# Performance work log

Measured on AMD Instinct MI355X. Metric: run time of the kernel, lower is better.

The kernel has to match this reference:

```python
import jax, jax.numpy as jnp
import numpy as np

NUM_LAYERS = 4


def setup_inputs() -> dict:
    key = jax.random.key(0)
    k1, k2, k3, k4 = jax.random.split(key, 4)
    num_users, num_items, D, E = 100000, 50000, 64, 2000000
    N = num_users + num_items
    emb_users = jax.random.normal(k1, (num_users, D), dtype=jnp.float32)
    emb_items = jax.random.normal(k2, (num_items, D), dtype=jnp.float32)
    src = jax.random.randint(k3, (E,), 0, N, dtype=jnp.int64)
    dst = jax.random.randint(k4, (E,), 0, N, dtype=jnp.int64)
    edge_index = jnp.stack([src, dst], axis=0)
    return {"emb_users": emb_users, "emb_items": emb_items, "edge_index": edge_index}


def _lightgcn(emb_users, emb_items, edge_index):
    num_users = emb_users.shape[0]
    num_items = emb_items.shape[0]
    N = num_users + num_items
    src, dst = edge_index[0], edge_index[1]

    # gcn_norm without self-loops (PyG LGConv default): deg over destination nodes
    ones = jnp.ones(src.shape[0], dtype=emb_users.dtype)
    deg = jax.ops.segment_sum(ones, dst, num_segments=N)
    deg_inv_sqrt = jnp.where(deg > 0, jax.lax.rsqrt(jnp.maximum(deg, 1.0)), 0.0)
    norm = deg_inv_sqrt[src] * deg_inv_sqrt[dst]  # [E]

    emb = jnp.concatenate([emb_users, emb_items], axis=0)  # [N, D]
    acc = emb
    for _ in range(NUM_LAYERS):
        msg = norm[:, None] * emb[src]  # [E, D]
        emb = jax.ops.segment_sum(msg, dst, num_segments=N)
        acc = acc + emb

    # original: 1/(L+1) * mean(stack, dim=1) == sum / (L+1)^2
    emb_final = acc / float((NUM_LAYERS + 1) ** 2)
    return emb_final[:num_users], emb_final[num_users:]


def reference(emb_users, emb_items, edge_index):
    return _lightgcn(emb_users, emb_items, edge_index)
```

## Files before the change

kernel.cpp:

```cpp
#include <hip/hip_runtime.h>
#include <hip/hip_bf16.h>

#define D 64
#define NUM_LAYERS 4
#define TILE 4096
#define EPT 16
#define BKMAX 320


__global__ void cnt_kernel(const int* __restrict__ dst, int* __restrict__ cnt, int E) {
    int e = blockIdx.x * blockDim.x + threadIdx.x;
    if (e < E) atomicAdd(&cnt[dst[e]], 1);
}

__global__ void dis_kernel(const int* __restrict__ cnt, float* __restrict__ dis, int N) {
    int i = blockIdx.x * blockDim.x + threadIdx.x;
    if (i < N) {
        int c = cnt[i];
        dis[i] = (c > 0) ? rsqrtf((float)c) : 0.0f;
    }
}

__global__ void scan1_kernel(const int* __restrict__ cnt, int* __restrict__ excl,
                             int* __restrict__ partials, int N) {
    __shared__ int sm[256];
    int i = blockIdx.x * 256 + threadIdx.x;
    int v = (i < N) ? cnt[i] : 0;
    sm[threadIdx.x] = v;
    __syncthreads();
    for (int ofs = 1; ofs < 256; ofs <<= 1) {
        int t = (threadIdx.x >= ofs) ? sm[threadIdx.x - ofs] : 0;
        __syncthreads();
        sm[threadIdx.x] += t;
        __syncthreads();
    }
    if (i < N) excl[i] = sm[threadIdx.x] - v;
    if (threadIdx.x == 255) partials[blockIdx.x] = sm[255];
}

__global__ void scan2_kernel(int* __restrict__ partials, int nb) {
    __shared__ int sm[1024];
    int v = (threadIdx.x < nb) ? partials[threadIdx.x] : 0;
    sm[threadIdx.x] = v;
    __syncthreads();
    for (int ofs = 1; ofs < 1024; ofs <<= 1) {
        int t = (threadIdx.x >= ofs) ? sm[threadIdx.x - ofs] : 0;
        __syncthreads();
        sm[threadIdx.x] += t;
        __syncthreads();
    }
    if (threadIdx.x < nb) partials[threadIdx.x] = sm[threadIdx.x] - v;
}

__global__ void scan3_kernel(int* __restrict__ row_start, const int* __restrict__ partials,
                             int N, int E) {
    int i = blockIdx.x * 256 + threadIdx.x;
    if (i < N) row_start[i] += partials[blockIdx.x];
    if (i == 0) row_start[N] = E;
}

__global__ void gcur_init_kernel(const int* __restrict__ row_start, int* __restrict__ gcur, int nbk) {
    int b = blockIdx.x * blockDim.x + threadIdx.x;
    if (b < nbk) gcur[b] = row_start[b << 9];
}


__global__ __launch_bounds__(256) void placeA_kernel(const int* __restrict__ src,
                                                     const int* __restrict__ dst,
                                                     const float* __restrict__ dis,
                                                     int* __restrict__ gcur,
                                                     int2* __restrict__ mid,
                                                     int E, int nbk) {
    __shared__ int hist[BKMAX];
    __shared__ int gbase[BKMAX];
    int t = threadIdx.x;
    int tile0 = blockIdx.x * TILE;
    for (int i = t; i < nbk; i += 256) hist[i] = 0;
    __syncthreads();

    int   p_[EPT];
    float w_[EPT];
    int   b_[EPT];
    int   r_[EPT];
#pragma unroll
    for (int i = 0; i < EPT; ++i) {
        int e = tile0 + i * 256 + t;
        b_[i] = -1;
        if (e < E) {
            int s = src[e], d = dst[e];
            p_[i] = s | ((d & 511) << 18);
            w_[i] = dis[s] * dis[d];
            b_[i] = d >> 9;
            r_[i] = atomicAdd(&hist[b_[i]], 1);
        }
    }
    __syncthreads();
    for (int b = t; b < nbk; b += 256) {
        int h = hist[b];
        gbase[b] = (h > 0) ? atomicAdd(&gcur[b], h) : 0;
    }
    __syncthreads();
#pragma unroll
    for (int i = 0; i < EPT; ++i) {
        if (b_[i] >= 0) {
            int pos = gbase[b_[i]] + r_[i];
            mid[pos] = make_int2(p_[i], __float_as_int(w_[i]));
        }
    }
}

__global__ __launch_bounds__(256) void placeB_kernel(const int* __restrict__ row_start,
                                                     const int2* __restrict__ mid,
                                                     int2* __restrict__ csr,
                                                     int N, int nbk) {
    __shared__ int cur[512];
    int b = blockIdx.x;
    int t = threadIdx.x;
    int node0 = b << 9;
    int nend = min(512, N - node0);
    for (int i = t; i < nend; i += 256) cur[i] = row_start[node0 + i];
    __syncthreads();
    int lo = row_start[node0];
    int hi = row_start[min(node0 + 512, N)];
    for (int e = lo + t; e < hi; e += 256) {
        int2 m = mid[e];
        int ldst = (m.x >> 18) & 511;
        int s = m.x & 0x3FFFF;
        int slot = atomicAdd(&cur[ldst], 1);
        csr[slot] = make_int2(s, m.y);
    }
}


__global__ void init_kernel(const float* __restrict__ users, const float* __restrict__ items,
                            unsigned* __restrict__ A, int nu_elems, int total2) {
    int i = blockIdx.x * blockDim.x + threadIdx.x;
    if (i >= total2) return;
    int base = i * 2;
    float2 v;
    if (base < nu_elems) v = ((const float2*)users)[i];
    else                 v = ((const float2*)items)[(base - nu_elems) >> 1];
    __hip_bfloat16 bx = __float2bfloat16(v.x);
    __hip_bfloat16 by = __float2bfloat16(v.y);
    unsigned p = (unsigned)(*reinterpret_cast<unsigned short*>(&bx))
               | ((unsigned)(*reinterpret_cast<unsigned short*>(&by)) << 16);
    A[i] = p;
}

__device__ __forceinline__ float bf_lo(unsigned u) { return __uint_as_float(u << 16); }
__device__ __forceinline__ float bf_hi(unsigned u) { return __uint_as_float(u & 0xffff0000u); }
__device__ __forceinline__ unsigned bf_pack(float x, float y) {
    __hip_bfloat16 bx = __float2bfloat16(x);
    __hip_bfloat16 by = __float2bfloat16(y);
    return (unsigned)(*reinterpret_cast<unsigned short*>(&bx))
         | ((unsigned)(*reinterpret_cast<unsigned short*>(&by)) << 16);
}

template <int FINAL>
__global__ void gather_kernel(const int* __restrict__ row_start,
                              const int2* __restrict__ csr,
                              const uint2* __restrict__ Au,
                              uint2* __restrict__ Bu,
                              const float* __restrict__ users, const float* __restrict__ items,
                              const uint2* __restrict__ L1u, const uint2* __restrict__ L2u,
                              float* __restrict__ out,
                              int N, int nu) {
    int node = (blockIdx.x * blockDim.x + threadIdx.x) >> 6;
    if (node >= N) return;
    int lane = threadIdx.x & 63;
    int q = lane >> 4;
    int c = lane & 15;
    int beg = row_start[node];
    int end = row_start[node + 1];
    int deg = end - beg;
    float ax = 0.0f, ay = 0.0f, az = 0.0f, aw = 0.0f;

    for (int base = 0; base < deg; base += 64) {
        int chunk = min(64, deg - base);
        int   sl = 0;
        float wl = 0.0f;
        if (lane < chunk) {
            int2 e = csr[beg + base + lane];
            sl = e.x;
            wl = __int_as_float(e.y);
        }
        int k = 0;
        for (; k + 8 <= chunk; k += 8) {
            int i0 = k + q, i1 = k + 4 + q;
            int   s0 = __shfl(sl, i0), s1 = __shfl(sl, i1);
            float w0 = __shfl(wl, i0), w1 = __shfl(wl, i1);
            uint2 u0 = Au[(size_t)s0 * 16 + c];
            uint2 u1 = Au[(size_t)s1 * 16 + c];
            ax += w0 * bf_lo(u0.x); ay += w0 * bf_hi(u0.x);
            az += w0 * bf_lo(u0.y); aw += w0 * bf_hi(u0.y);
            ax += w1 * bf_lo(u1.x); ay += w1 * bf_hi(u1.x);
            az += w1 * bf_lo(u1.y); aw += w1 * bf_hi(u1.y);
        }
        for (; k < chunk; k += 4) {
            int i0 = k + q;
            int   s = __shfl(sl, i0);
            float w = __shfl(wl, i0);
            uint2 u = Au[(size_t)s * 16 + c];
            ax += w * bf_lo(u.x); ay += w * bf_hi(u.x);
            az += w * bf_lo(u.y); aw += w * bf_hi(u.y);
        }
    }

    ax += __shfl_xor(ax, 16); ay += __shfl_xor(ay, 16);
    az += __shfl_xor(az, 16); aw += __shfl_xor(aw, 16);
    ax += __shfl_xor(ax, 32); ay += __shfl_xor(ay, 32);
    az += __shfl_xor(az, 32); aw += __shfl_xor(aw, 32);

    if (q == 0) {
        size_t ro = (size_t)node * 16 + c;
        if (FINAL) {
            uint2 l1 = L1u[ro], l2 = L2u[ro], l3 = Au[ro];
            float4 e0;
            if (node < nu) e0 = ((const float4*)users)[ro];
            else           e0 = ((const float4*)items)[(size_t)(node - nu) * 16 + c];
            float rx = (e0.x + bf_lo(l1.x) + bf_lo(l2.x) + bf_lo(l3.x) + ax) * 0.04f;
            float ry = (e0.y + bf_hi(l1.x) + bf_hi(l2.x) + bf_hi(l3.x) + ay) * 0.04f;
            float rz = (e0.z + bf_lo(l1.y) + bf_lo(l2.y) + bf_lo(l3.y) + az) * 0.04f;
            float rw = (e0.w + bf_hi(l1.y) + bf_hi(l2.y) + bf_hi(l3.y) + aw) * 0.04f;
            ((float4*)out)[ro] = make_float4(rx, ry, rz, rw);
        } else {
            uint2 p;
            p.x = bf_pack(ax, ay);
            p.y = bf_pack(az, aw);
            Bu[ro] = p;
        }
    }
}


extern "C" void kernel_launch(void* const* d_in, const int* in_sizes, int n_in,
                              void* d_out, int out_size, void* d_ws, size_t ws_size,
                              hipStream_t stream) {
    const float* users = (const float*)d_in[0];
    const float* items = (const float*)d_in[1];
    const int*   eidx  = (const int*)d_in[2];

    const int nu = in_sizes[0] / D;
    const int ni = in_sizes[1] / D;
    const int N  = nu + ni;
    const int E  = in_sizes[2] / 2;
    const int Nf = N * D;
    const int nbk = (N + 511) >> 9;

    const int* src = eidx;
    const int* dst = eidx + E;

    char* ws = (char*)d_ws;
    size_t off = 0;
    auto alloc = [&](size_t bytes) {
        char* p = ws + off;
        off += (bytes + 255) & ~(size_t)255;
        return p;
    };
    int*   cnt       = (int*)alloc((size_t)N * 4);
    float* dis       = (float*)alloc((size_t)N * 4);
    int*   row_start = (int*)alloc((size_t)(N + 1) * 4);
    int*   partials  = (int*)alloc(1024 * 4);
    int*   gcur      = (int*)alloc(512 * 4);
    int2*  csr       = (int2*)alloc((size_t)E * 8);
    unsigned* A0 = (unsigned*)alloc((size_t)Nf * 2);
    unsigned* L1 = (unsigned*)alloc((size_t)Nf * 2);
    unsigned* L2 = (unsigned*)alloc((size_t)Nf * 2);
    unsigned* L3 = (unsigned*)alloc((size_t)Nf * 2);
    int2* mid = (int2*)L3;

    const int B256 = 256;
    auto blocks = [](long long n, int b) { return (int)((n + b - 1) / b); };
    const int nbN = blocks(N, B256);

    hipMemsetAsync(cnt, 0, (size_t)N * 4, stream);
    cnt_kernel<<<blocks(E, B256), B256, 0, stream>>>(dst, cnt, E);
    dis_kernel<<<nbN, B256, 0, stream>>>(cnt, dis, N);

    scan1_kernel<<<nbN, B256, 0, stream>>>(cnt, row_start, partials, N);
    scan2_kernel<<<1, 1024, 0, stream>>>(partials, nbN);
    scan3_kernel<<<nbN, B256, 0, stream>>>(row_start, partials, N, E);
    gcur_init_kernel<<<blocks(nbk, B256), B256, 0, stream>>>(row_start, gcur, nbk);

    placeA_kernel<<<blocks(E, TILE), B256, 0, stream>>>(src, dst, dis, gcur, mid, E, nbk);
    placeB_kernel<<<nbk, B256, 0, stream>>>(row_start, mid, csr, N, nbk);

    init_kernel<<<blocks(Nf / 2, B256), B256, 0, stream>>>(users, items, A0, nu * D, Nf / 2);

    const int ggrid = blocks(N, B256 / 64);
    gather_kernel<0><<<ggrid, B256, 0, stream>>>(row_start, csr, (const uint2*)A0, (uint2*)L1,
                                                 nullptr, nullptr, nullptr, nullptr, nullptr, N, nu);
    gather_kernel<0><<<ggrid, B256, 0, stream>>>(row_start, csr, (const uint2*)L1, (uint2*)L2,
                                                 nullptr, nullptr, nullptr, nullptr, nullptr, N, nu);
    gather_kernel<0><<<ggrid, B256, 0, stream>>>(row_start, csr, (const uint2*)L2, (uint2*)L3,
                                                 nullptr, nullptr, nullptr, nullptr, nullptr, N, nu);
    gather_kernel<1><<<ggrid, B256, 0, stream>>>(row_start, csr, (const uint2*)L3, nullptr,
                                                 users, items, (const uint2*)L1, (const uint2*)L2,
                                                 (float*)d_out, N, nu);
}
```

Measured before the change: 464.9 us.

## Build CSR from bucket histogram, computing degrees and norms inside bucket passes

The per-node global atomic degree count and three-kernel global scan are replaced by a shared-memory bucket histogram plus a single-block bucket scan. Per-node degrees, row starts and inverse-sqrt norms are now computed inside a per-bucket pass (placeB1) using shared-memory atomics and a local scan. Edge weights are computed in the final placement (placeB2) instead of in placeA, which lets the intermediate buffer hold 4-byte packed entries instead of 8-byte pairs. The aim is fewer kernel launches and less global atomic and memory traffic during preprocessing, at the cost of one extra read pass over the intermediate array.

```diff
diff --git a/kernel.cpp b/kernel.cpp
--- a/kernel.cpp
+++ b/kernel.cpp
@@ -8,68 +8,42 @@
 #define BKMAX 320
 
 
-__global__ void cnt_kernel(const int* __restrict__ dst, int* __restrict__ cnt, int E) {
-    int e = blockIdx.x * blockDim.x + threadIdx.x;
-    if (e < E) atomicAdd(&cnt[dst[e]], 1);
-}
-
-__global__ void dis_kernel(const int* __restrict__ cnt, float* __restrict__ dis, int N) {
-    int i = blockIdx.x * blockDim.x + threadIdx.x;
-    if (i < N) {
-        int c = cnt[i];
-        dis[i] = (c > 0) ? rsqrtf((float)c) : 0.0f;
-    }
-}
-
-__global__ void scan1_kernel(const int* __restrict__ cnt, int* __restrict__ excl,
-                             int* __restrict__ partials, int N) {
-    __shared__ int sm[256];
-    int i = blockIdx.x * 256 + threadIdx.x;
-    int v = (i < N) ? cnt[i] : 0;
-    sm[threadIdx.x] = v;
-    __syncthreads();
-    for (int ofs = 1; ofs < 256; ofs <<= 1) {
-        int t = (threadIdx.x >= ofs) ? sm[threadIdx.x - ofs] : 0;
+__global__ void bhist_kernel(const int* __restrict__ dst, int* __restrict__ bcnt, int E, int nbk) {
+    __shared__ int h[BKMAX];
+    for (int i = threadIdx.x; i < nbk; i += blockDim.x) h[i] = 0;
+    __syncthreads();
+    int stride = gridDim.x * blockDim.x;
+    for (int e = blockIdx.x * blockDim.x + threadIdx.x; e < E; e += stride)
+        atomicAdd(&h[dst[e] >> 9], 1);
+    __syncthreads();
+    for (int i = threadIdx.x; i < nbk; i += blockDim.x)
+        if (h[i] > 0) atomicAdd(&bcnt[i], h[i]);
+}
+
+__global__ __launch_bounds__(512) void bscan_kernel(const int* __restrict__ bcnt,
+                                                    int* __restrict__ bstart,
+                                                    int* __restrict__ gcur, int nbk, int E) {
+    __shared__ int sm[512];
+    int t = threadIdx.x;
+    int v = (t < nbk) ? bcnt[t] : 0;
+    sm[t] = v;
+    __syncthreads();
+    for (int ofs = 1; ofs < 512; ofs <<= 1) {
+        int x = (t >= ofs) ? sm[t - ofs] : 0;
         __syncthreads();
-        sm[threadIdx.x] += t;
+        sm[t] += x;
         __syncthreads();
     }
-    if (i < N) excl[i] = sm[threadIdx.x] - v;
-    if (threadIdx.x == 255) partials[blockIdx.x] = sm[255];
-}
-
-__global__ void scan2_kernel(int* __restrict__ partials, int nb) {
-    __shared__ int sm[1024];
-    int v = (threadIdx.x < nb) ? partials[threadIdx.x] : 0;
-    sm[threadIdx.x] = v;
-    __syncthreads();
-    for (int ofs = 1; ofs < 1024; ofs <<= 1) {
-        int t = (threadIdx.x >= ofs) ? sm[threadIdx.x - ofs] : 0;
-        __syncthreads();
-        sm[threadIdx.x] += t;
-        __syncthreads();
-    }
-    if (threadIdx.x < nb) partials[threadIdx.x] = sm[threadIdx.x] - v;
-}
-
-__global__ void scan3_kernel(int* __restrict__ row_start, const int* __restrict__ partials,
-                             int N, int E) {
-    int i = blockIdx.x * 256 + threadIdx.x;
-    if (i < N) row_start[i] += partials[blockIdx.x];
-    if (i == 0) row_start[N] = E;
-}
-
-__global__ void gcur_init_kernel(const int* __restrict__ row_start, int* __restrict__ gcur, int nbk) {
-    int b = blockIdx.x * blockDim.x + threadIdx.x;
-    if (b < nbk) gcur[b] = row_start[b << 9];
+    int excl = sm[t] - v;
+    if (t < nbk) { bstart[t] = excl; gcur[t] = excl; }
+    if (t == 0) bstart[nbk] = E;
 }
 
 
 __global__ __launch_bounds__(256) void placeA_kernel(const int* __restrict__ src,
                                                      const int* __restrict__ dst,
-                                                     const float* __restrict__ dis,
                                                      int* __restrict__ gcur,
-                                                     int2* __restrict__ mid,
+                                                     int* __restrict__ mid,
                                                      int E, int nbk) {
     __shared__ int hist[BKMAX];
     __shared__ int gbase[BKMAX];
@@ -78,10 +52,9 @@
     for (int i = t; i < nbk; i += 256) hist[i] = 0;
     __syncthreads();
 
-    int   p_[EPT];
-    float w_[EPT];
-    int   b_[EPT];
-    int   r_[EPT];
+    int p_[EPT];
+    int b_[EPT];
+    int r_[EPT];
 #pragma unroll
     for (int i = 0; i < EPT; ++i) {
         int e = tile0 + i * 256 + t;
@@ -89,7 +62,6 @@
         if (e < E) {
             int s = src[e], d = dst[e];
             p_[i] = s | ((d & 511) << 18);
-            w_[i] = dis[s] * dis[d];
             b_[i] = d >> 9;
             r_[i] = atomicAdd(&hist[b_[i]], 1);
         }
@@ -102,32 +74,66 @@
     __syncthreads();
 #pragma unroll
     for (int i = 0; i < EPT; ++i) {
-        if (b_[i] >= 0) {
-            int pos = gbase[b_[i]] + r_[i];
-            mid[pos] = make_int2(p_[i], __float_as_int(w_[i]));
-        }
-    }
-}
-
-__global__ __launch_bounds__(256) void placeB_kernel(const int* __restrict__ row_start,
-                                                     const int2* __restrict__ mid,
-                                                     int2* __restrict__ csr,
-                                                     int N, int nbk) {
-    __shared__ int cur[512];
+        if (b_[i] >= 0) mid[gbase[b_[i]] + r_[i]] = p_[i];
+    }
+}
+
+__global__ __launch_bounds__(512) void placeB1_kernel(const int* __restrict__ bstart,
+                                                      const int* __restrict__ mid,
+                                                      int* __restrict__ row_start,
+                                                      float* __restrict__ dis,
+                                                      int N, int nbk, int E) {
+    __shared__ int degsm[512];
+    __shared__ int sc[512];
     int b = blockIdx.x;
     int t = threadIdx.x;
     int node0 = b << 9;
-    int nend = min(512, N - node0);
-    for (int i = t; i < nend; i += 256) cur[i] = row_start[node0 + i];
-    __syncthreads();
-    int lo = row_start[node0];
-    int hi = row_start[min(node0 + 512, N)];
-    for (int e = lo + t; e < hi; e += 256) {
-        int2 m = mid[e];
-        int ldst = (m.x >> 18) & 511;
-        int s = m.x & 0x3FFFF;
-        int slot = atomicAdd(&cur[ldst], 1);
-        csr[slot] = make_int2(s, m.y);
+    int lo = bstart[b], hi = bstart[b + 1];
+    degsm[t] = 0;
+    __syncthreads();
+    for (int e = lo + t; e < hi; e += 512)
+        atomicAdd(&degsm[(mid[e] >> 18) & 511], 1);
+    __syncthreads();
+    int d = degsm[t];
+    sc[t] = d;
+    __syncthreads();
+    for (int ofs = 1; ofs < 512; ofs <<= 1) {
+        int x = (t >= ofs) ? sc[t - ofs] : 0;
+        __syncthreads();
+        sc[t] += x;
+        __syncthreads();
+    }
+    int excl = sc[t] - d;
+    int node = node0 + t;
+    if (node < N) {
+        row_start[node] = lo + excl;
+        dis[node] = (d > 0) ? rsqrtf((float)d) : 0.0f;
+    }
+    if (b == nbk - 1 && t == 0) row_start[N] = E;
+}
+
+__global__ __launch_bounds__(512) void placeB2_kernel(const int* __restrict__ bstart,
+                                                      const int* __restrict__ mid,
+                                                      const int* __restrict__ row_start,
+                                                      const float* __restrict__ dis,
+                                                      int2* __restrict__ csr, int N) {
+    __shared__ int cur[512];
+    __shared__ float dloc[512];
+    int b = blockIdx.x;
+    int t = threadIdx.x;
+    int node0 = b << 9;
+    int node = node0 + t;
+    if (node < N) { cur[t] = row_start[node]; dloc[t] = dis[node]; }
+    else          { cur[t] = 0; dloc[t] = 0.0f; }
+    __syncthreads();
+    int lo = bstart[b], hi = bstart[b + 1];
+    for (int e = lo + t; e < hi; e += 512) {
+        int m = mid[e];
+        int l = (m >> 18) & 511;
+        int s = m & 0x3FFFF;
+        float w = dis[s] * dloc[l];
+        int slot = atomicAdd(&cur[l], 1);
+        csr[slot] = make_int2(s, __float_as_int(w));
     }
 }
 
@@ -257,33 +263,28 @@
         off += (bytes + 255) & ~(size_t)255;
         return p;
     };
-    int*   cnt       = (int*)alloc((size_t)N * 4);
     float* dis       = (float*)alloc((size_t)N * 4);
     int*   row_start = (int*)alloc((size_t)(N + 1) * 4);
-    int*   partials  = (int*)alloc(1024 * 4);
-    int*   gcur      = (int*)alloc(512 * 4);
+    int*   bcnt      = (int*)alloc(BKMAX * 4);
+    int*   bstart    = (int*)alloc((BKMAX + 1) * 4);
+    int*   gcur      = (int*)alloc(BKMAX * 4);
     int2*  csr       = (int2*)alloc((size_t)E * 8);
     unsigned* A0 = (unsigned*)alloc((size_t)Nf * 2);
     unsigned* L1 = (unsigned*)alloc((size_t)Nf * 2);
     unsigned* L2 = (unsigned*)alloc((size_t)Nf * 2);
     unsigned* L3 = (unsigned*)alloc((size_t)Nf * 2);
-    int2* mid = (int2*)L3;
+    int* mid = (int*)L3;
 
     const int B256 = 256;
     auto blocks = [](long long n, int b) { return (int)((n + b - 1) / b); };
-    const int nbN = blocks(N, B256);
-
-    hipMemsetAsync(cnt, 0, (size_t)N * 4, stream);
-    cnt_kernel<<<blocks(E, B256), B256, 0, stream>>>(dst, cnt, E);
-    dis_kernel<<<nbN, B256, 0, stream>>>(cnt, dis, N);
-
-    scan1_kernel<<<nbN, B256, 0, stream>>>(cnt, row_start, partials, N);
-    scan2_kernel<<<1, 1024, 0, stream>>>(partials, nbN);
-    scan3_kernel<<<nbN, B256, 0, stream>>>(row_start, partials, N, E);
-    gcur_init_kernel<<<blocks(nbk, B256), B256, 0, stream>>>(row_start, gcur, nbk);
-
-    placeA_kernel<<<blocks(E, TILE), B256, 0, stream>>>(src, dst, dis, gcur, mid, E, nbk);
-    placeB_kernel<<<nbk, B256, 0, stream>>>(row_start, mid, csr, N, nbk);
+
+    hipMemsetAsync(bcnt, 0, BKMAX * 4, stream);
+    bhist_kernel<<<1024, B256, 0, stream>>>(dst, bcnt, E, nbk);
+    bscan_kernel<<<1, 512, 0, stream>>>(bcnt, bstart, gcur, nbk, E);
+
+    placeA_kernel<<<blocks(E, TILE), B256, 0, stream>>>(src, dst, gcur, mid, E, nbk);
+    placeB1_kernel<<<nbk, 512, 0, stream>>>(bstart, mid, row_start, dis, N, nbk, E);
+    placeB2_kernel<<<nbk, 512, 0, stream>>>(bstart, mid, row_start, dis, csr, N);
 
     init_kernel<<<blocks(Nf / 2, B256), B256, 0, stream>>>(users, items, A0, nu * D, Nf / 2);
 
```

After: 402.7 us. 13.4% less time.
